# Performance work log

Measured on AMD Instinct MI355X. Metric: run time of the kernel, lower is better.

## Reference

```python
import jax, jax.numpy as jnp
import numpy as np

NUM_HEADS = 8
D_MODEL = 256
DIM = D_MODEL // NUM_HEADS  # 32
EPS = 1e-6


def _proj(x, W, b):
    # Conv1d with kernel_size=1 == channel-mixing matmul over length axis
    return jnp.einsum('oi,bil->bol', W, x) + b[None, :, None]


def _linear_attention(q, k, v):
    # q,k,v: [B, dim, heads, L]
    q = jax.nn.elu(q) + 1.0
    k = jax.nn.elu(k) + 1.0
    L = v.shape[3]
    v = v / L
    # KV: [B, dim_v, dim_k, heads]
    KV = jnp.einsum('bdhm,bqhm->bqdh', k, v)
    # Z: [B, heads, L]
    Z = 1.0 / (jnp.einsum('bdhm,bdh->bhm', q, k.sum(3)) + EPS)
    # out: [B, dim, heads, L]
    return jnp.einsum('bdhm,bqdh,bhm->bqhm', q, KV, Z) * L


def setup_inputs() -> dict:
    key = jax.random.key(0)
    ks = jax.random.split(key, 11)
    B, L = 8, 4096
    s = 0.05
    return {
        'query': jax.random.normal(ks[0], (B, D_MODEL, L), dtype=jnp.float32),
        'key':   jax.random.normal(ks[1], (B, D_MODEL, L), dtype=jnp.float32),
        'value': jax.random.normal(ks[2], (B, D_MODEL, L), dtype=jnp.float32),
        'Wq': jax.random.normal(ks[3], (D_MODEL, D_MODEL), dtype=jnp.float32) * s,
        'bq': jnp.zeros((D_MODEL,), dtype=jnp.float32),
        'Wk': jax.random.normal(ks[4], (D_MODEL, D_MODEL), dtype=jnp.float32) * s,
        'bk': jnp.zeros((D_MODEL,), dtype=jnp.float32),
        'Wv': jax.random.normal(ks[5], (D_MODEL, D_MODEL), dtype=jnp.float32) * s,
        'bv': jnp.zeros((D_MODEL,), dtype=jnp.float32),
        'Wm': jax.random.normal(ks[6], (D_MODEL, D_MODEL), dtype=jnp.float32) * s,
        'bm': jnp.zeros((D_MODEL,), dtype=jnp.float32),
    }


def reference(query, key, value, Wq, bq, Wk, bk, Wv, bv, Wm, bm):
    B = query.shape[0]
    q = _proj(query, Wq, bq).reshape(B, DIM, NUM_HEADS, -1)
    k = _proj(key,   Wk, bk).reshape(B, DIM, NUM_HEADS, -1)
    v = _proj(value, Wv, bv).reshape(B, DIM, NUM_HEADS, -1)
    x = _linear_attention(q, k, v)           # [B, dim, heads, L]
    x = x.reshape(B, D_MODEL, -1)            # merge heads back to channels
    return jnp.einsum('oi,bil->bol', Wm, x) + bm[None, :, None]
```

## Files before the change

kernel.cpp:

```cpp
#include <hip/hip_runtime.h>
#include <math.h>

#define D_MODEL 256
#define NHEADS 8
#define HDIM 32
#define BATCH 8
#define SEQL 4096
#define EPS 1e-6f

typedef _Float16 f16;
typedef _Float16 f16x4 __attribute__((ext_vector_type(4)));
typedef _Float16 f16x8 __attribute__((ext_vector_type(8)));
typedef float f32x4 __attribute__((ext_vector_type(4)));

__device__ __forceinline__ float elu1(float x) {
    return x > 0.f ? x + 1.f : __expf(x);
}

__global__ void prep_kernel(const float* __restrict__ Wq, const float* __restrict__ Wk,
                            const float* __restrict__ Wv, const float* __restrict__ Wm,
                            const float* __restrict__ bq, const float* __restrict__ bk,
                            const float* __restrict__ bv,
                            f16* __restrict__ w16, float* __restrict__ bperm) {
    if (blockIdx.x < 1024) {
        int idx = blockIdx.x * 256 + threadIdx.x;
        int mat = idx >> 16, r = (idx >> 8) & 255, c = idx & 255;
        const float* W = (mat == 0) ? Wq : (mat == 1) ? Wk : (mat == 2) ? Wv : Wm;
        float v;
        if (mat < 3) v = W[(size_t)(((r & 31) << 3) + (r >> 5)) * 256 + c];
        else         v = W[(size_t)r * 256 + (((c & 31) << 3) + (c >> 5))];
        w16[idx] = (f16)v;
    } else {
        int t = threadIdx.x;
        bperm[0 * 256 + t] = bq[((t & 31) << 3) + (t >> 5)];
        bperm[1 * 256 + t] = bk[((t & 31) << 3) + (t >> 5)];
        bperm[2 * 256 + t] = bv[((t & 31) << 3) + (t >> 5)];
    }
}

__global__ void zero_kernel(float* __restrict__ p, int n) {
    int i = blockIdx.x * blockDim.x + threadIdx.x;
    if (i < n) p[i] = 0.f;
}

#define BSTR 40
__global__ __launch_bounds__(256, 4) void gemm_stage1(
    const float* __restrict__ Xq, const float* __restrict__ Xk, const float* __restrict__ Xv,
    const f16* __restrict__ w16, const float* __restrict__ bperm,
    f16* __restrict__ yq, f16* __restrict__ yk, f16* __restrict__ yv) {
    __shared__ __align__(16) char smem[18432];
    f16* Bs = (f16*)smem;
    f16* Cb = (f16*)smem;

    const int z = blockIdx.z;
    const int which = z >> 3;
    const int b = z & 7;
    const float* X = (which == 0) ? Xq : (which == 1) ? Xk : Xv;
    const f16* W = w16 + which * 65536;
    f16* Y = (which == 0) ? yq : (which == 1) ? yk : yv;
    const float* bp = bperm + which * 256;

    const int l0 = blockIdx.x * 128;
    const int m0 = blockIdx.y * 128;
    const int tid = threadIdx.x;
    const int wave = tid >> 6, lane = tid & 63;
    const int wm = wave >> 1, wn = wave & 1;
    const int ln = lane & 15, quad = lane >> 4;
    const int bp8 = tid & 7;
    const int bg = tid >> 3;

    f32x4 acc[4][4];
#pragma unroll
    for (int mf = 0; mf < 4; ++mf)
#pragma unroll
        for (int nf = 0; nf < 4; ++nf)
#pragma unroll
            for (int r = 0; r < 4; ++r) acc[mf][nf][r] = 0.f;

    for (int k0 = 0; k0 < D_MODEL; k0 += 32) {
        __syncthreads();
        {
            const float* xb = X + ((size_t)b * D_MODEL + k0 + 4 * bp8) * SEQL + l0 + 4 * bg;
            float4 r0 = *(const float4*)(xb + 0 * SEQL);
            float4 r1 = *(const float4*)(xb + 1 * SEQL);
            float4 r2 = *(const float4*)(xb + 2 * SEQL);
            float4 r3 = *(const float4*)(xb + 3 * SEQL);
            f16x4 w;
            w[0] = (f16)r0.x; w[1] = (f16)r1.x; w[2] = (f16)r2.x; w[3] = (f16)r3.x;
            *(f16x4*)&Bs[(4 * bg + 0) * BSTR + 4 * bp8] = w;
            w[0] = (f16)r0.y; w[1] = (f16)r1.y; w[2] = (f16)r2.y; w[3] = (f16)r3.y;
            *(f16x4*)&Bs[(4 * bg + 1) * BSTR + 4 * bp8] = w;
            w[0] = (f16)r0.z; w[1] = (f16)r1.z; w[2] = (f16)r2.z; w[3] = (f16)r3.z;
            *(f16x4*)&Bs[(4 * bg + 2) * BSTR + 4 * bp8] = w;
            w[0] = (f16)r0.w; w[1] = (f16)r1.w; w[2] = (f16)r2.w; w[3] = (f16)r3.w;
            *(f16x4*)&Bs[(4 * bg + 3) * BSTR + 4 * bp8] = w;
        }
        __syncthreads();
        f16x8 af[4], bf[4];
#pragma unroll
        for (int mf = 0; mf < 4; ++mf)
            af[mf] = *(const f16x8*)(W + (size_t)(m0 + wm * 64 + mf * 16 + ln) * 256 + k0 + quad * 8);
#pragma unroll
        for (int nf = 0; nf < 4; ++nf)
            bf[nf] = *(const f16x8*)&Bs[(wn * 64 + nf * 16 + ln) * BSTR + quad * 8];
#pragma unroll
        for (int mf = 0; mf < 4; ++mf)
#pragma unroll
            for (int nf = 0; nf < 4; ++nf)
                acc[mf][nf] = __builtin_amdgcn_mfma_f32_16x16x32_f16(af[mf], bf[nf], acc[mf][nf], 0, 0, 0);
    }
    float bv_[4][4];
#pragma unroll
    for (int mf = 0; mf < 4; ++mf)
#pragma unroll
        for (int r = 0; r < 4; ++r)
            bv_[mf][r] = bp[m0 + wm * 64 + mf * 16 + quad * 4 + r];
#pragma unroll
    for (int pass = 0; pass < 2; ++pass) {
        __syncthreads();
        if (wm == pass) {
#pragma unroll
            for (int mf = 0; mf < 4; ++mf)
#pragma unroll
                for (int nf = 0; nf < 4; ++nf) {
                    const int olocal = mf * 16 + quad * 4;
                    const int llocal = wn * 64 + nf * 16 + ln;
                    f16x4 w;
#pragma unroll
                    for (int r = 0; r < 4; ++r) w[r] = (f16)(acc[mf][nf][r] + bv_[mf][r]);
                    *(f16x4*)&Cb[llocal * 72 + olocal] = w;
                }
        }
        __syncthreads();
        const int l = tid >> 1, half = tid & 1;
        f16* yr = Y + ((size_t)(b * SEQL + l0 + l)) * 256 + m0 + pass * 64 + half * 32;
#pragma unroll
        for (int c = 0; c < 4; ++c)
            *(f16x8*)(yr + c * 8) = *(const f16x8*)&Cb[l * 72 + half * 32 + c * 8];
    }
}

__global__ __launch_bounds__(256) void kv_kernel(
    const f16* __restrict__ kp, const f16* __restrict__ vp,
    float* __restrict__ KV, float* __restrict__ ksum) {
    const int bh = blockIdx.y;
    const int b = bh >> 3, h = bh & 7;
    const int lbase = blockIdx.x * (SEQL / 16);
    __shared__ float ks[64][33];
    __shared__ float vs[64][33];
    const int t = threadIdx.x;
    const int lrow = t >> 2, seg = t & 3;
    const int kd = t & 31, qg = t >> 5;
    float a0 = 0.f, a1 = 0.f, a2 = 0.f, a3 = 0.f, ss = 0.f;
    for (int lc = 0; lc < SEQL / 16; lc += 64) {
        __syncthreads();
        const size_t off = ((size_t)(b * SEQL + lbase + lc + lrow)) * 256 + h * 32 + seg * 8;
        f16x8 k8 = *(const f16x8*)(kp + off);
        f16x8 v8 = *(const f16x8*)(vp + off);
#pragma unroll
        for (int j = 0; j < 8; ++j) {
            ks[lrow][seg * 8 + j] = elu1((float)k8[j]);
            vs[lrow][seg * 8 + j] = (float)v8[j];
        }
        __syncthreads();
#pragma unroll 8
        for (int li = 0; li < 64; ++li) {
            const float kk = ks[li][kd];
            ss += kk;
            a0 += kk * vs[li][qg * 4 + 0];
            a1 += kk * vs[li][qg * 4 + 1];
            a2 += kk * vs[li][qg * 4 + 2];
            a3 += kk * vs[li][qg * 4 + 3];
        }
    }
    float* KVb = KV + (size_t)(b * NHEADS + h) * HDIM * HDIM;
    atomicAdd(&KVb[(qg * 4 + 0) * HDIM + kd], a0);
    atomicAdd(&KVb[(qg * 4 + 1) * HDIM + kd], a1);
    atomicAdd(&KVb[(qg * 4 + 2) * HDIM + kd], a2);
    atomicAdd(&KVb[(qg * 4 + 3) * HDIM + kd], a3);
    if (qg == 0) atomicAdd(&ksum[(size_t)(b * NHEADS + h) * HDIM + kd], ss);
}

__global__ __launch_bounds__(256) void attn_out_kernel(
    const f16* __restrict__ qp, const float* __restrict__ KV,
    const float* __restrict__ ksum, const f16* __restrict__ wm16,
    const float* __restrict__ bm, float* __restrict__ out) {
    __shared__ __align__(16) f16 xs[64 * 264];
    __shared__ __align__(16) f16 Baug[8 * 48 * 40];
    __shared__ float dens[8][64];
    const int b = blockIdx.y;
    const int l0 = blockIdx.x * 64;
    const int t = threadIdx.x;
    const int wave = t >> 6, lane = t & 63;
    const int ln = lane & 15, quad = lane >> 4;

    {
        const int h = t >> 5, qd = t & 31;
        const float* kvp = KV + ((size_t)(b * NHEADS + h) * HDIM + qd) * HDIM;
        f16* dst = &Baug[(h * 48 + qd) * 40];
#pragma unroll
        for (int i = 0; i < 32; i += 4) {
            float4 a = *(const float4*)(kvp + i);
            f16x4 w4;
            w4[0] = (f16)a.x; w4[1] = (f16)a.y; w4[2] = (f16)a.z; w4[3] = (f16)a.w;
            *(f16x4*)(dst + i) = w4;
        }
        Baug[(h * 48 + 32) * 40 + qd] = (f16)ksum[(size_t)(b * NHEADS + h) * HDIM + qd];
    }
    {
        const int row = t & 63, cg = t >> 6;
        const f16* qr = qp + ((size_t)(b * SEQL + l0 + row)) * 256 + cg * 64;
        f16* dst = &xs[row * 264 + cg * 64];
#pragma unroll
        for (int u = 0; u < 64; u += 8) {
            f16x8 v = *(const f16x8*)(qr + u);
            f16x8 w;
#pragma unroll
            for (int j = 0; j < 8; ++j) w[j] = (f16)elu1((float)v[j]);
            *(f16x8*)(dst + u) = w;
        }
    }
    __syncthreads();
#pragma unroll
    for (int hh = 0; hh < 2; ++hh) {
        const int h = wave * 2 + hh;
        f16x8 a_s[4], b_s[3];
#pragma unroll
        for (int mf = 0; mf < 4; ++mf)
            a_s[mf] = *(const f16x8*)&xs[(mf * 16 + ln) * 264 + h * 32 + quad * 8];
#pragma unroll
        for (int nf = 0; nf < 3; ++nf)
            b_s[nf] = *(const f16x8*)&Baug[(h * 48 + nf * 16 + ln) * 40 + quad * 8];
        f32x4 C[4][3];
#pragma unroll
        for (int mf = 0; mf < 4; ++mf)
#pragma unroll
            for (int nf = 0; nf < 3; ++nf) {
#pragma unroll
                for (int r = 0; r < 4; ++r) C[mf][nf][r] = 0.f;
                C[mf][nf] = __builtin_amdgcn_mfma_f32_16x16x32_f16(a_s[mf], b_s[nf], C[mf][nf], 0, 0, 0);
            }
        if (ln == 0) {
#pragma unroll
            for (int mf = 0; mf < 4; ++mf)
#pragma unroll
                for (int r = 0; r < 4; ++r)
                    dens[h][mf * 16 + quad * 4 + r] = C[mf][2][r];
        }
        __syncthreads();
#pragma unroll
        for (int mf = 0; mf < 4; ++mf)
#pragma unroll
            for (int r = 0; r < 4; ++r) {
                const int l = mf * 16 + quad * 4 + r;
                const float rd = __builtin_amdgcn_rcpf(dens[h][l] + EPS);
#pragma unroll
                for (int nf = 0; nf < 2; ++nf)
                    xs[l * 264 + h * 32 + nf * 16 + ln] = (f16)(C[mf][nf][r] * rd);
            }
        __syncthreads();
    }
    f32x4 acc[4][4];
#pragma unroll
    for (int mf = 0; mf < 4; ++mf)
#pragma unroll
        for (int nf = 0; nf < 4; ++nf)
#pragma unroll
            for (int r = 0; r < 4; ++r) acc[mf][nf][r] = 0.f;
    for (int k0 = 0; k0 < D_MODEL; k0 += 32) {
        f16x8 af[4], bf[4];
#pragma unroll
        for (int mf = 0; mf < 4; ++mf)
            af[mf] = *(const f16x8*)(wm16 + (size_t)(wave * 64 + mf * 16 + ln) * 256 + k0 + quad * 8);
#pragma unroll
        for (int nf = 0; nf < 4; ++nf)
            bf[nf] = *(const f16x8*)&xs[(nf * 16 + ln) * 264 + k0 + quad * 8];
#pragma unroll
        for (int mf = 0; mf < 4; ++mf)
#pragma unroll
            for (int nf = 0; nf < 4; ++nf)
                acc[mf][nf] = __builtin_amdgcn_mfma_f32_16x16x32_f16(af[mf], bf[nf], acc[mf][nf], 0, 0, 0);
    }
#pragma unroll
    for (int mf = 0; mf < 4; ++mf) {
        const int o = wave * 64 + mf * 16 + quad * 4;
#pragma unroll
        for (int r = 0; r < 4; ++r) {
            const float bb = bm[o + r];
            float* op = out + ((size_t)(b * D_MODEL + o + r)) * SEQL + l0;
#pragma unroll
            for (int nf = 0; nf < 4; ++nf)
                op[nf * 16 + ln] = acc[mf][nf][r] + bb;
        }
    }
}

extern "C" void kernel_launch(void* const* d_in, const int* in_sizes, int n_in,
                              void* d_out, int out_size, void* d_ws, size_t ws_size,
                              hipStream_t stream) {
    const float* query = (const float*)d_in[0];
    const float* key_  = (const float*)d_in[1];
    const float* value = (const float*)d_in[2];
    const float* Wq = (const float*)d_in[3];
    const float* bq = (const float*)d_in[4];
    const float* Wk = (const float*)d_in[5];
    const float* bk = (const float*)d_in[6];
    const float* Wv = (const float*)d_in[7];
    const float* bv = (const float*)d_in[8];
    const float* Wm = (const float*)d_in[9];
    const float* bm = (const float*)d_in[10];

    char* w = (char*)d_ws;
    f16*   w16   = (f16*)w;
    float* bperm = (float*)(w + 524288);
    float* KV    = (float*)(w + 528384);
    float* ksum  = (float*)(w + 790528);
    f16*   qp    = (f16*)(w + 802816);
    f16*   kp    = qp + (size_t)BATCH * SEQL * 256;
    f16*   vp    = kp + (size_t)BATCH * SEQL * 256;

    prep_kernel<<<1025, 256, 0, stream>>>(Wq, Wk, Wv, Wm, bq, bk, bv, w16, bperm);
    zero_kernel<<<(65536 + 2048 + 255) / 256, 256, 0, stream>>>(KV, 65536 + 2048);

    gemm_stage1<<<dim3(SEQL / 128, 2, 24), 256, 0, stream>>>(
        query, key_, value, w16, bperm, qp, kp, vp);

    kv_kernel<<<dim3(16, BATCH * NHEADS), 256, 0, stream>>>(kp, vp, KV, ksum);

    attn_out_kernel<<<dim3(SEQL / 64, BATCH), 256, 0, stream>>>(
        qp, KV, ksum, w16 + 3 * 65536, bm, (float*)d_out);
}
```

Baseline: 233.3 us.

## Double-buffer stage-1 GEMM K loop and halve output-channel tile

Restructures the projection GEMM to prefetch the next K slice of inputs and weights into registers while computing on the current shared-memory buffer, using two LDS buffers. The output-channel tile is halved to 64, doubling the grid and cutting accumulators per thread, which should improve occupancy and latency hiding. The cost is that each input tile is now read from global memory by twice as many blocks, increasing input traffic.

```diff
diff --git a/kernel.cpp b/kernel.cpp
--- a/kernel.cpp
+++ b/kernel.cpp
@@ -48,8 +48,8 @@
     const float* __restrict__ Xq, const float* __restrict__ Xk, const float* __restrict__ Xv,
     const f16* __restrict__ w16, const float* __restrict__ bperm,
     f16* __restrict__ yq, f16* __restrict__ yk, f16* __restrict__ yv) {
-    __shared__ __align__(16) char smem[18432];
-    f16* Bs = (f16*)smem;
+    __shared__ __align__(16) char smem[20480];
+    f16* BsBuf[2] = {(f16*)smem, (f16*)smem + 128 * BSTR};
     f16* Cb = (f16*)smem;
 
     const int z = blockIdx.z;
@@ -61,7 +61,7 @@
     const float* bp = bperm + which * 256;
 
     const int l0 = blockIdx.x * 128;
-    const int m0 = blockIdx.y * 128;
+    const int m0 = blockIdx.y * 64;
     const int tid = threadIdx.x;
     const int wave = tid >> 6, lane = tid & 63;
     const int wm = wave >> 1, wn = wave & 1;
@@ -69,74 +69,95 @@
     const int bp8 = tid & 7;
     const int bg = tid >> 3;
 
-    f32x4 acc[4][4];
-#pragma unroll
-    for (int mf = 0; mf < 4; ++mf)
+    const float* Xbase = X + ((size_t)b * D_MODEL + 4 * bp8) * SEQL + l0 + 4 * bg;
+    const f16* Wbase0 = W + (size_t)(m0 + wm * 32 + 0 * 16 + ln) * 256 + quad * 8;
+    const f16* Wbase1 = W + (size_t)(m0 + wm * 32 + 1 * 16 + ln) * 256 + quad * 8;
+
+    float4 xr[4];
+    f16x8 af[2][2];
+
+#define LOADX(K0) do { \
+        const float* xb_ = Xbase + (size_t)(K0) * SEQL; \
+        xr[0] = *(const float4*)(xb_ + 0 * SEQL); \
+        xr[1] = *(const float4*)(xb_ + 1 * SEQL); \
+        xr[2] = *(const float4*)(xb_ + 2 * SEQL); \
+        xr[3] = *(const float4*)(xb_ + 3 * SEQL); \
+    } while (0)
+
+#define STOREB(BUF) do { \
+        f16* Bsb_ = BsBuf[BUF]; \
+        f16x4 w_; \
+        w_[0] = (f16)xr[0].x; w_[1] = (f16)xr[1].x; w_[2] = (f16)xr[2].x; w_[3] = (f16)xr[3].x; \
+        *(f16x4*)&Bsb_[(4 * bg + 0) * BSTR + 4 * bp8] = w_; \
+        w_[0] = (f16)xr[0].y; w_[1] = (f16)xr[1].y; w_[2] = (f16)xr[2].y; w_[3] = (f16)xr[3].y; \
+        *(f16x4*)&Bsb_[(4 * bg + 1) * BSTR + 4 * bp8] = w_; \
+        w_[0] = (f16)xr[0].z; w_[1] = (f16)xr[1].z; w_[2] = (f16)xr[2].z; w_[3] = (f16)xr[3].z; \
+        *(f16x4*)&Bsb_[(4 * bg + 2) * BSTR + 4 * bp8] = w_; \
+        w_[0] = (f16)xr[0].w; w_[1] = (f16)xr[1].w; w_[2] = (f16)xr[2].w; w_[3] = (f16)xr[3].w; \
+        *(f16x4*)&Bsb_[(4 * bg + 3) * BSTR + 4 * bp8] = w_; \
+    } while (0)
+
+    f32x4 acc[2][4];
+#pragma unroll
+    for (int mf = 0; mf < 2; ++mf)
 #pragma unroll
         for (int nf = 0; nf < 4; ++nf)
 #pragma unroll
             for (int r = 0; r < 4; ++r) acc[mf][nf][r] = 0.f;
 
-    for (int k0 = 0; k0 < D_MODEL; k0 += 32) {
-        __syncthreads();
-        {
-            const float* xb = X + ((size_t)b * D_MODEL + k0 + 4 * bp8) * SEQL + l0 + 4 * bg;
-            float4 r0 = *(const float4*)(xb + 0 * SEQL);
-            float4 r1 = *(const float4*)(xb + 1 * SEQL);
-            float4 r2 = *(const float4*)(xb + 2 * SEQL);
-            float4 r3 = *(const float4*)(xb + 3 * SEQL);
+    LOADX(0);
+    af[0][0] = *(const f16x8*)(Wbase0 + 0);
+    af[0][1] = *(const f16x8*)(Wbase1 + 0);
+    STOREB(0);
+    __syncthreads();
+
+#pragma unroll
+    for (int it = 0; it < 8; ++it) {
+        const int k0 = it * 32;
+        const int cur = it & 1, nxt = cur ^ 1;
+        if (it < 7) {
+            LOADX(k0 + 32);
+            af[nxt][0] = *(const f16x8*)(Wbase0 + k0 + 32);
+            af[nxt][1] = *(const f16x8*)(Wbase1 + k0 + 32);
+        }
+        f16x8 bf[4];
+        const f16* Bsc = BsBuf[cur];
+#pragma unroll
+        for (int nf = 0; nf < 4; ++nf)
+            bf[nf] = *(const f16x8*)&Bsc[(wn * 64 + nf * 16 + ln) * BSTR + quad * 8];
+#pragma unroll
+        for (int mf = 0; mf < 2; ++mf)
+#pragma unroll
+            for (int nf = 0; nf < 4; ++nf)
+                acc[mf][nf] = __builtin_amdgcn_mfma_f32_16x16x32_f16(af[cur][mf], bf[nf], acc[mf][nf], 0, 0, 0);
+        if (it < 7) STOREB(nxt);
+        __syncthreads();
+    }
+
+    float bv_[2][4];
+#pragma unroll
+    for (int mf = 0; mf < 2; ++mf)
+#pragma unroll
+        for (int r = 0; r < 4; ++r)
+            bv_[mf][r] = bp[m0 + wm * 32 + mf * 16 + quad * 4 + r];
+#pragma unroll
+    for (int mf = 0; mf < 2; ++mf)
+#pragma unroll
+        for (int nf = 0; nf < 4; ++nf) {
+            const int olocal = wm * 32 + mf * 16 + quad * 4;
+            const int llocal = wn * 64 + nf * 16 + ln;
             f16x4 w;
-            w[0] = (f16)r0.x; w[1] = (f16)r1.x; w[2] = (f16)r2.x; w[3] = (f16)r3.x;
-            *(f16x4*)&Bs[(4 * bg + 0) * BSTR + 4 * bp8] = w;
-            w[0] = (f16)r0.y; w[1] = (f16)r1.y; w[2] = (f16)r2.y; w[3] = (f16)r3.y;
-            *(f16x4*)&Bs[(4 * bg + 1) * BSTR + 4 * bp8] = w;
-            w[0] = (f16)r0.z; w[1] = (f16)r1.z; w[2] = (f16)r2.z; w[3] = (f16)r3.z;
-            *(f16x4*)&Bs[(4 * bg + 2) * BSTR + 4 * bp8] = w;
-            w[0] = (f16)r0.w; w[1] = (f16)r1.w; w[2] = (f16)r2.w; w[3] = (f16)r3.w;
-            *(f16x4*)&Bs[(4 * bg + 3) * BSTR + 4 * bp8] = w;
-        }
-        __syncthreads();
-        f16x8 af[4], bf[4];
-#pragma unroll
-        for (int mf = 0; mf < 4; ++mf)
-            af[mf] = *(const f16x8*)(W + (size_t)(m0 + wm * 64 + mf * 16 + ln) * 256 + k0 + quad * 8);
-#pragma unroll
-        for (int nf = 0; nf < 4; ++nf)
-            bf[nf] = *(const f16x8*)&Bs[(wn * 64 + nf * 16 + ln) * BSTR + quad * 8];
-#pragma unroll
-        for (int mf = 0; mf < 4; ++mf)
-#pragma unroll
-            for (int nf = 0; nf < 4; ++nf)
-                acc[mf][nf] = __builtin_amdgcn_mfma_f32_16x16x32_f16(af[mf], bf[nf], acc[mf][nf], 0, 0, 0);
-    }
-    float bv_[4][4];
-#pragma unroll
-    for (int mf = 0; mf < 4; ++mf)
-#pragma unroll
-        for (int r = 0; r < 4; ++r)
-            bv_[mf][r] = bp[m0 + wm * 64 + mf * 16 + quad * 4 + r];
-#pragma unroll
-    for (int pass = 0; pass < 2; ++pass) {
-        __syncthreads();
-        if (wm == pass) {
-#pragma unroll
-            for (int mf = 0; mf < 4; ++mf)
-#pragma unroll
-                for (int nf = 0; nf < 4; ++nf) {
-                    const int olocal = mf * 16 + quad * 4;
-                    const int llocal = wn * 64 + nf * 16 + ln;
-                    f16x4 w;
-#pragma unroll
-                    for (int r = 0; r < 4; ++r) w[r] = (f16)(acc[mf][nf][r] + bv_[mf][r]);
-                    *(f16x4*)&Cb[llocal * 72 + olocal] = w;
-                }
-        }
-        __syncthreads();
+#pragma unroll
+            for (int r = 0; r < 4; ++r) w[r] = (f16)(acc[mf][nf][r] + bv_[mf][r]);
+            *(f16x4*)&Cb[llocal * 72 + olocal] = w;
+        }
+    __syncthreads();
+    {
         const int l = tid >> 1, half = tid & 1;
-        f16* yr = Y + ((size_t)(b * SEQL + l0 + l)) * 256 + m0 + pass * 64 + half * 32;
-#pragma unroll
-        for (int c = 0; c < 4; ++c)
-            *(f16x8*)(yr + c * 8) = *(const f16x8*)&Cb[l * 72 + half * 32 + c * 8];
+        f16* yr = Y + ((size_t)(b * SEQL + l0 + l)) * 256 + m0 + half * 32;
+#pragma unroll
+        for (int u = 0; u < 4; ++u)
+            *(f16x8*)(yr + u * 8) = *(const f16x8*)&Cb[l * 72 + half * 32 + u * 8];
     }
 }
 
@@ -322,7 +343,7 @@
     prep_kernel<<<1025, 256, 0, stream>>>(Wq, Wk, Wv, Wm, bq, bk, bv, w16, bperm);
     zero_kernel<<<(65536 + 2048 + 255) / 256, 256, 0, stream>>>(KV, 65536 + 2048);
 
-    gemm_stage1<<<dim3(SEQL / 128, 2, 24), 256, 0, stream>>>(
+    gemm_stage1<<<dim3(SEQL / 128, 4, 24), 256, 0, stream>>>(
         query, key_, value, w16, bperm, qp, kp, vp);
 
     kv_kernel<<<dim3(16, BATCH * NHEADS), 256, 0, stream>>>(kp, vp, KV, ksum);
```

Result: slower. 244.5 us (+4.8%).
